# Optimization experiments

Measured on AMD Instinct MI355X. Metric: run time of the kernel, lower is better.

## Reference

```python
import jax, jax.numpy as jnp
import numpy as np

B, W, N, F_IN = 2, 8, 10000, 5
E = 80000
H = 128


def setup_inputs() -> dict:
    key = jax.random.key(0)
    ks = jax.random.split(key, 16)
    s = 0.05
    inp = {
        "x": jax.random.normal(ks[0], (B, W, N, F_IN), dtype=jnp.float32),
        "edge_index": jax.random.randint(ks[1], (2, E), 0, N, dtype=jnp.int64),
        # GCN layer 1 (in_features -> hidden) and layer 2 (hidden -> hidden)
        "gcn1_w": jax.random.normal(ks[2], (F_IN, H), dtype=jnp.float32) * s,
        "gcn1_b": jnp.zeros((H,), dtype=jnp.float32),
        "gcn2_w": jax.random.normal(ks[3], (H, H), dtype=jnp.float32) * s,
        "gcn2_b": jnp.zeros((H,), dtype=jnp.float32),
        # LSTM (torch gate order: i, f, g, o)
        "lstm_w_ih": jax.random.normal(ks[4], (4 * H, H), dtype=jnp.float32) * s,
        "lstm_w_hh": jax.random.normal(ks[5], (4 * H, H), dtype=jnp.float32) * s,
        "lstm_b_ih": jnp.zeros((4 * H,), dtype=jnp.float32),
        "lstm_b_hh": jnp.zeros((4 * H,), dtype=jnp.float32),
        # Decoder MLP: H -> H//2 -> 1
        "dec_w1": jax.random.normal(ks[6], (H, H // 2), dtype=jnp.float32) * s,
        "dec_b1": jnp.zeros((H // 2,), dtype=jnp.float32),
        "dec_w2": jax.random.normal(ks[7], (H // 2, 1), dtype=jnp.float32) * s,
        "dec_b2": jnp.zeros((1,), dtype=jnp.float32),
    }
    return inp


def _forward(x, edge_index, gcn1_w, gcn1_b, gcn2_w, gcn2_b,
             lstm_w_ih, lstm_w_hh, lstm_b_ih, lstm_b_hh,
             dec_w1, dec_b1, dec_w2, dec_b2):
    b, w, n, f_in = x.shape
    h_dim = gcn1_w.shape[1]
    # --- GCN normalization (PyG GCNConv default: add self-loops, sym-norm) ---
    loop = jnp.arange(n, dtype=edge_index.dtype)
    src = jnp.concatenate([edge_index[0], loop])
    dst = jnp.concatenate([edge_index[1], loop])
    deg = jnp.zeros((n,), x.dtype).at[dst].add(jnp.float32(1.0))
    dinv = jax.lax.rsqrt(deg)
    norm = dinv[src] * dinv[dst]  # (E+N,)

    def gcn(h, wm, bias):
        # h: (BW, N, Fin) -> (BW, N, H). Transform-then-aggregate (linear op).
        ht = h @ wm                                   # (BW, N, H)
        msg = ht[:, src, :] * norm[None, :, None]      # (BW, E+N, H)
        agg = jnp.zeros_like(ht).at[:, dst, :].add(msg)
        return agg + bias

    xf = x.reshape(b * w, n, f_in)
    h = jax.nn.relu(gcn(xf, gcn1_w, gcn1_b))   # dropout is identity at eval
    h = jax.nn.relu(gcn(h, gcn2_w, gcn2_b))

    # (BW, N, H) -> (B, N, W, H) -> (B*N, W, H): per-node temporal sequences
    h = h.reshape(b, w, n, h_dim).transpose(0, 2, 1, 3).reshape(b * n, w, h_dim)

    # --- single-layer LSTM, keep only last hidden state ---
    def step(carry, xt):
        hp, cp = carry
        gates = xt @ lstm_w_ih.T + hp @ lstm_w_hh.T + lstm_b_ih + lstm_b_hh
        i, f, g, o = jnp.split(gates, 4, axis=-1)
        c = jax.nn.sigmoid(f) * cp + jax.nn.sigmoid(i) * jnp.tanh(g)
        hn = jax.nn.sigmoid(o) * jnp.tanh(c)
        return (hn, c), None

    init = (jnp.zeros((b * n, h_dim), x.dtype), jnp.zeros((b * n, h_dim), x.dtype))
    (h_last, _), _ = jax.lax.scan(step, init, h.transpose(1, 0, 2))  # scan over W

    # --- MLP decoder ---
    d = jax.nn.relu(h_last @ dec_w1 + dec_b1)
    pred = (d @ dec_w2 + dec_b2)[..., 0]
    return pred.reshape(b, n)


def reference(x, edge_index, gcn1_w, gcn1_b, gcn2_w, gcn2_b,
              lstm_w_ih, lstm_w_hh, lstm_b_ih, lstm_b_hh,
              dec_w1, dec_b1, dec_w2, dec_b2):
    return _forward(x, edge_index, gcn1_w, gcn1_b, gcn2_w, gcn2_b,
                    lstm_w_ih, lstm_w_hh, lstm_b_ih, lstm_b_hh,
                    dec_w1, dec_b1, dec_w2, dec_b2)
```

## Files before the change

### kernel.cpp

```cpp
#include <hip/hip_runtime.h>
#include <hip/hip_fp16.h>
#include <cstdint>
#include <cstddef>

#define Bn   2
#define Wn   8
#define Nn   10000
#define Fin  5
#define En   80000
#define Hn   128
#define BWn  (Bn*Wn)
#define ROWS (BWn*Nn)
#define MR   (Bn*Nn)
#define LROWS 32

typedef _Float16 half8 __attribute__((ext_vector_type(8)));
typedef float f32x4 __attribute__((ext_vector_type(4)));

#define LOG2E 1.44269504088896f

__device__ __forceinline__ float fast_sigmoid(float x) {
    return __builtin_amdgcn_rcpf(1.f + __builtin_amdgcn_exp2f(-LOG2E * x));
}
__device__ __forceinline__ float fast_tanh(float x) {
    return fmaf(-2.f, __builtin_amdgcn_rcpf(1.f + __builtin_amdgcn_exp2f(2.f * LOG2E * x)), 1.f);
}


__global__ void init_counts_kernel(int* counts) {
    int i = blockIdx.x * blockDim.x + threadIdx.x;
    if (i < Nn) counts[i] = 1;
}

__global__ void count_edges_kernel(const int* __restrict__ ei, int* counts) {
    int e = blockIdx.x * blockDim.x + threadIdx.x;
    if (e < En) atomicAdd(&counts[ei[En + e]], 1);
}

enum { CHUNK = 10 };
static_assert(CHUNK * 1024 >= Nn, "scan chunk");

__global__ __launch_bounds__(1024) void scan_kernel(
    const int* __restrict__ counts, int* __restrict__ row_ptr,
    int* __restrict__ fill_ptr, float* __restrict__ dinv) {
    __shared__ int sums[1024];
    const int t = threadIdx.x;
    const int base = t * CHUNK;
    int cnt[CHUNK];
    int s = 0;
    #pragma unroll
    for (int i = 0; i < CHUNK; ++i) {
        int idx = base + i;
        int v = (idx < Nn) ? counts[idx] : 0;
        cnt[i] = v; s += v;
    }
    sums[t] = s;
    __syncthreads();
    for (int off = 1; off < 1024; off <<= 1) {
        int v = (t >= off) ? sums[t - off] : 0;
        __syncthreads();
        sums[t] += v;
        __syncthreads();
    }
    int excl = (t == 0) ? 0 : sums[t - 1];
    #pragma unroll
    for (int i = 0; i < CHUNK; ++i) {
        int idx = base + i;
        if (idx < Nn) {
            row_ptr[idx] = excl;
            fill_ptr[idx] = excl;
            dinv[idx] = rsqrtf((float)cnt[i]);
            excl += cnt[i];
        }
    }
    if (t == 1023) row_ptr[Nn] = excl;
}

__global__ void fill_kernel(const int* __restrict__ ei,
                            const float* __restrict__ dinv,
                            int* fill_ptr, int* __restrict__ col,
                            float* __restrict__ wgt) {
    int i = blockIdx.x * blockDim.x + threadIdx.x;
    if (i < Nn) {
        int p = atomicAdd(&fill_ptr[i], 1);
        col[p] = i;
        wgt[p] = dinv[i] * dinv[i];
    } else if (i < Nn + En) {
        int e = i - Nn;
        int s = ei[e];
        int d = ei[En + e];
        int p = atomicAdd(&fill_ptr[d], 1);
        col[p] = s;
        wgt[p] = dinv[s] * dinv[d];
    }
}


__global__ void bsum_kernel(const float* __restrict__ a, const float* __restrict__ b,
                            float* __restrict__ out) {
    int i = blockIdx.x * blockDim.x + threadIdx.x;
    if (i < 4 * Hn) out[i] = a[i] + b[i];
}

__global__ void convert_w_kernel(const float* __restrict__ wih, const float* __restrict__ whh,
                                 const float* __restrict__ g2w,
                                 _Float16* __restrict__ wif, _Float16* __restrict__ whf,
                                 _Float16* __restrict__ g2wt) {
    int i = blockIdx.x * blockDim.x + threadIdx.x;
    if (i < 131072) {
        int idx = i & 65535;
        int j = idx & 7, lane = (idx >> 3) & 63, kt = (idx >> 9) & 3, ct = idx >> 11;
        int n = ct * 16 + (lane & 15);
        int k = kt * 32 + (lane >> 4) * 8 + j;
        if (i < 65536) wif[idx] = (_Float16)wih[n * 128 + k];
        else           whf[idx] = (_Float16)whh[n * 128 + k];
    } else if (i < 131072 + 16384) {
        int j = i - 131072;
        int n = j >> 7, k = j & 127;
        g2wt[j] = (_Float16)g2w[k * Hn + n];
    }
}

__global__ __launch_bounds__(128) void agg_x_kernel(
    const float* __restrict__ x, const int* __restrict__ row_ptr,
    const int* __restrict__ col, const float* __restrict__ wgt,
    float* __restrict__ aggx) {
    const int n = blockIdx.x;
    const int t = threadIdx.x;
    const int s = t >> 3, f = t & 7;
    if (f >= Fin) return;
    const int start = row_ptr[n], end = row_ptr[n + 1];
    float acc = 0.f;
    for (int e = start; e < end; ++e) {
        int c = col[e];
        acc = fmaf(wgt[e], x[((size_t)s * Nn + c) * Fin + f], acc);
    }
    aggx[((size_t)n * BWn + s) * Fin + f] = acc;
}

__global__ __launch_bounds__(256) void gcn2_fused_kernel(
    const float* __restrict__ aggx, const float* __restrict__ w1,
    const float* __restrict__ b1, const _Float16* __restrict__ g2wt,
    _Float16* __restrict__ C) {
    __shared__ __align__(16) _Float16 s_buf[128][136];
    __shared__ _Float16 Bs[128][40];
    const int tid = threadIdx.x;
    const int m0 = blockIdx.x * 128;
    {
        const int rg = tid >> 4;
        const int cg = tid & 15;
        float wreg[Fin][8], breg[8];
        #pragma unroll
        for (int k = 0; k < 8; ++k) breg[k] = b1[cg * 8 + k];
        #pragma unroll
        for (int f = 0; f < Fin; ++f)
            #pragma unroll
            for (int k = 0; k < 8; ++k) wreg[f][k] = w1[f * Hn + cg * 8 + k];
        #pragma unroll
        for (int rr = 0; rr < 8; ++rr) {
            const float* ar = aggx + (size_t)(m0 + rg * 8 + rr) * Fin;
            float a[Fin];
            #pragma unroll
            for (int f = 0; f < Fin; ++f) a[f] = ar[f];
            half8 v;
            #pragma unroll
            for (int k = 0; k < 8; ++k) {
                float s = breg[k];
                #pragma unroll
                for (int f = 0; f < Fin; ++f) s = fmaf(a[f], wreg[f][k], s);
                v[k] = (_Float16)fmaxf(s, 0.f);
            }
            *(half8*)&s_buf[rg * 8 + rr][cg * 8] = v;
        }
    }
    __syncthreads();
    const int wave = tid >> 6, lane = tid & 63;
    const int l = lane & 15, q = lane >> 4;
    const int wm = (wave & 1) * 64, wn = (wave >> 1) * 64;
    f32x4 acc[4][4];
    #pragma unroll
    for (int i = 0; i < 4; ++i)
        #pragma unroll
        for (int j = 0; j < 4; ++j) acc[i][j] = (f32x4){0.f, 0.f, 0.f, 0.f};
    for (int kt = 0; kt < 128; kt += 32) {
        #pragma unroll
        for (int j = 0; j < 2; ++j) {
            int idx = tid + j * 256;
            int r = idx >> 2, c = (idx & 3) * 8;
            *(half8*)&Bs[r][c] = *(const half8*)(g2wt + (size_t)r * 128 + kt + c);
        }
        __syncthreads();
        half8 af[4], bf[4];
        #pragma unroll
        for (int i = 0; i < 4; ++i) af[i] = *(const half8*)&s_buf[wm + i * 16 + l][kt + q * 8];
        #pragma unroll
        for (int j = 0; j < 4; ++j) bf[j] = *(const half8*)&Bs[wn + j * 16 + l][q * 8];
        #pragma unroll
        for (int i = 0; i < 4; ++i)
            #pragma unroll
            for (int j = 0; j < 4; ++j)
                acc[i][j] = __builtin_amdgcn_mfma_f32_16x16x32_f16(
                    af[i], bf[j], acc[i][j], 0, 0, 0);
        __syncthreads();
    }
    #pragma unroll
    for (int j = 0; j < 4; ++j) {
        int ccol = wn + j * 16 + l;
        #pragma unroll
        for (int i = 0; i < 4; ++i)
            #pragma unroll
            for (int r = 0; r < 4; ++r)
                s_buf[wm + i * 16 + q * 4 + r][ccol] = (_Float16)acc[i][j][r];
    }
    __syncthreads();
    const size_t base = (size_t)m0 * 128;
    #pragma unroll
    for (int it = 0; it < 8; ++it) {
        int idx = it * 256 + tid;
        int row = idx >> 4, ch = (idx & 15) * 8;
        *(half8*)(C + base + (size_t)row * 128 + ch) = *(const half8*)&s_buf[row][ch];
    }
}

__global__ __launch_bounds__(256) void gcn_agg2_kernel(
    const _Float16* __restrict__ ht, const int* __restrict__ row_ptr,
    const int* __restrict__ col, const float* __restrict__ wgt,
    const float* __restrict__ bias, _Float16* __restrict__ out) {
    const int n = blockIdx.x;
    const int t = threadIdx.x;
    const int s = t >> 4;
    const int g = (t & 15) * 8;
    const int start = row_ptr[n], end = row_ptr[n + 1];
    float acc[8];
    #pragma unroll
    for (int j = 0; j < 8; ++j) acc[j] = 0.f;
    for (int e = start; e < end; ++e) {
        const int c = col[e];
        const float w = wgt[e];
        half8 v = *(const half8*)(ht + ((size_t)c * BWn + s) * Hn + g);
        #pragma unroll
        for (int j = 0; j < 8; ++j) acc[j] = fmaf(w, (float)v[j], acc[j]);
    }
    half8 o;
    #pragma unroll
    for (int j = 0; j < 8; ++j) o[j] = (_Float16)fmaxf(acc[j] + bias[g + j], 0.f);
    *(half8*)(out + ((size_t)n * BWn + s) * Hn + g) = o;
}

__global__ __launch_bounds__(512, 1) void lstm_fused2_kernel(
    const _Float16* __restrict__ h2, const _Float16* __restrict__ wif,
    const _Float16* __restrict__ whf, const float* __restrict__ bsum,
    _Float16* __restrict__ hf) {
    __shared__ __align__(16) _Float16 x_lds[2][LROWS][144];
    __shared__ __align__(16) _Float16 h_lds[LROWS][144];
    const int tid = threadIdx.x;
    const int nw = tid >> 6, lane = tid & 63;
    const int l = lane & 15, q = lane >> 4;
    const int r0 = blockIdx.x * LROWS;
    const int srow = tid >> 4, sch = (tid & 15) * 8;
    const int sgrow = r0 + srow;
    const int sb = (sgrow >= Nn) ? 1 : 0;
    const int sn = sgrow - sb * Nn;
    const _Float16* xbase = h2 + ((size_t)sn * BWn + sb * Wn) * 128 + sch;

    half8 wic[4][4], whc[4][4];
    #pragma unroll
    for (int g = 0; g < 4; ++g) {
        int ct = g * 8 + nw;
        #pragma unroll
        for (int kt = 0; kt < 4; ++kt) {
            wic[g][kt] = *(const half8*)(wif + (((size_t)ct * 4 + kt) * 64 + lane) * 8);
            whc[g][kt] = *(const half8*)(whf + (((size_t)ct * 4 + kt) * 64 + lane) * 8);
        }
    }
    float bias[4];
    #pragma unroll
    for (int g = 0; g < 4; ++g) bias[g] = bsum[g * 128 + nw * 16 + l];
    float c_reg[2][4];
    #pragma unroll
    for (int i = 0; i < 2; ++i)
        #pragma unroll
        for (int r = 0; r < 4; ++r) c_reg[i][r] = 0.f;

    *(half8*)&x_lds[0][srow][sch] = *(const half8*)(xbase);
    __syncthreads();

    for (int t = 0; t < Wn; ++t) {
        half8 xv = {0, 0, 0, 0, 0, 0, 0, 0};
        if (t + 1 < Wn) xv = *(const half8*)(xbase + (size_t)(t + 1) * 128);

        f32x4 acc[2][4];
        #pragma unroll
        for (int i = 0; i < 2; ++i)
            #pragma unroll
            for (int g = 0; g < 4; ++g)
                acc[i][g] = (f32x4){bias[g], bias[g], bias[g], bias[g]};

        #pragma unroll
        for (int kt = 0; kt < 4; ++kt) {
            half8 af[2];
            #pragma unroll
            for (int i = 0; i < 2; ++i)
                af[i] = *(const half8*)&x_lds[t & 1][i * 16 + l][kt * 32 + q * 8];
            #pragma unroll
            for (int i = 0; i < 2; ++i)
                #pragma unroll
                for (int g = 0; g < 4; ++g)
                    acc[i][g] = __builtin_amdgcn_mfma_f32_16x16x32_f16(
                        af[i], wic[g][kt], acc[i][g], 0, 0, 0);
        }
        if (t > 0) {
            #pragma unroll
            for (int kt = 0; kt < 4; ++kt) {
                half8 af[2];
                #pragma unroll
                for (int i = 0; i < 2; ++i)
                    af[i] = *(const half8*)&h_lds[i * 16 + l][kt * 32 + q * 8];
                #pragma unroll
                for (int i = 0; i < 2; ++i)
                    #pragma unroll
                    for (int g = 0; g < 4; ++g)
                        acc[i][g] = __builtin_amdgcn_mfma_f32_16x16x32_f16(
                            af[i], whc[g][kt], acc[i][g], 0, 0, 0);
            }
        }
        __syncthreads();

        #pragma unroll
        for (int i = 0; i < 2; ++i) {
            #pragma unroll
            for (int r = 0; r < 4; ++r) {
                float si = fast_sigmoid(acc[i][0][r]);
                float sf = fast_sigmoid(acc[i][1][r]);
                float tg = fast_tanh(acc[i][2][r]);
                float so = fast_sigmoid(acc[i][3][r]);
                float cn = sf * c_reg[i][r] + si * tg;
                c_reg[i][r] = cn;
                h_lds[i * 16 + q * 4 + r][nw * 16 + l] = (_Float16)(so * fast_tanh(cn));
            }
        }
        if (t + 1 < Wn) *(half8*)&x_lds[(t + 1) & 1][srow][sch] = xv;
        __syncthreads();
    }
    *(half8*)(hf + (size_t)sgrow * 128 + sch) = *(const half8*)&h_lds[srow][sch];
}

__global__ __launch_bounds__(256) void decoder_kernel(
    const _Float16* __restrict__ h, const float* __restrict__ w1,
    const float* __restrict__ b1, const float* __restrict__ w2,
    const float* __restrict__ b2, float* __restrict__ out) {
    const int wave = threadIdx.x >> 6;
    const int lane = threadIdx.x & 63;
    const int row = blockIdx.x * 4 + wave;
    if (row >= MR) return;
    const _Float16* hr = h + (size_t)row * Hn;
    float d = b1[lane];
    #pragma unroll 8
    for (int k = 0; k < Hn; ++k) d = fmaf((float)hr[k], w1[k * 64 + lane], d);
    d = fmaxf(d, 0.f);
    float p = d * w2[lane];
    #pragma unroll
    for (int off = 32; off; off >>= 1) p += __shfl_down(p, off);
    if (lane == 0) out[row] = p + b2[0];
}


extern "C" void kernel_launch(void* const* d_in, const int* in_sizes, int n_in,
                              void* d_out, int out_size, void* d_ws, size_t ws_size,
                              hipStream_t stream) {
    const float* x   = (const float*)d_in[0];
    const int*   ei  = (const int*)d_in[1];
    const float* g1w = (const float*)d_in[2];
    const float* g1b = (const float*)d_in[3];
    const float* g2w = (const float*)d_in[4];
    const float* g2b = (const float*)d_in[5];
    const float* wih = (const float*)d_in[6];
    const float* whh = (const float*)d_in[7];
    const float* bih = (const float*)d_in[8];
    const float* bhh = (const float*)d_in[9];
    const float* dw1 = (const float*)d_in[10];
    const float* db1 = (const float*)d_in[11];
    const float* dw2 = (const float*)d_in[12];
    const float* db2 = (const float*)d_in[13];
    float* out = (float*)d_out;

    char* p = (char*)d_ws;
    auto alloc = [&](size_t bytes) {
        char* r = p;
        p += (bytes + 255) & ~(size_t)255;
        return r;
    };
    int*      counts   = (int*)     alloc(Nn * 4);
    int*      row_ptr  = (int*)     alloc((Nn + 1) * 4);
    int*      fill_ptr = (int*)     alloc((Nn + 1) * 4);
    float*    dinv     = (float*)   alloc(Nn * 4);
    float*    bsum     = (float*)   alloc(4 * Hn * 4);
    int*      col      = (int*)     alloc((En + Nn) * 4);
    float*    wgt      = (float*)   alloc((En + Nn) * 4);
    _Float16* wif      = (_Float16*)alloc(512 * 128 * 2);
    _Float16* whf      = (_Float16*)alloc(512 * 128 * 2);
    _Float16* g2wt     = (_Float16*)alloc(128 * 128 * 2);
    float*    aggx     = (float*)   alloc((size_t)ROWS * Fin * 4);
    _Float16* htf      = (_Float16*)alloc((size_t)ROWS * Hn * 2);
    _Float16* h2f      = (_Float16*)alloc((size_t)ROWS * Hn * 2);
    _Float16* hf       = (_Float16*)alloc((size_t)MR * Hn * 2);

    init_counts_kernel<<<(Nn + 255) / 256, 256, 0, stream>>>(counts);
    count_edges_kernel<<<(En + 255) / 256, 256, 0, stream>>>(ei, counts);
    scan_kernel<<<1, 1024, 0, stream>>>(counts, row_ptr, fill_ptr, dinv);
    fill_kernel<<<(Nn + En + 255) / 256, 256, 0, stream>>>(ei, dinv, fill_ptr, col, wgt);
    bsum_kernel<<<(4 * Hn + 255) / 256, 256, 0, stream>>>(bih, bhh, bsum);
    convert_w_kernel<<<(131072 + 16384 + 255) / 256, 256, 0, stream>>>(
        wih, whh, g2w, wif, whf, g2wt);

    agg_x_kernel<<<Nn, 128, 0, stream>>>(x, row_ptr, col, wgt, aggx);

    gcn2_fused_kernel<<<ROWS / 128, 256, 0, stream>>>(aggx, g1w, g1b, g2wt, htf);

    gcn_agg2_kernel<<<Nn, 256, 0, stream>>>(htf, row_ptr, col, wgt, g2b, h2f);

    lstm_fused2_kernel<<<MR / LROWS, 512, 0, stream>>>(h2f, wif, whf, bsum, hf);

    decoder_kernel<<<(MR + 3) / 4, 256, 0, stream>>>(hf, dw1, db1, dw2, db2, out);
}
```

Baseline: 281.7 us.

## Merge setup kernels, transpose x node-major, fuse decoder into LSTM

Four small setup kernels (count init, edge counting, bias sum, weight conversion) become one multi-role setup_kernel plus a memset. The self-loop +1 now happens inside the scan. The setup kernel also transposes x into a node-major layout, so agg_x gathers one contiguous 80-float row per neighbour instead of 16 strided rows. The LSTM double-buffers h_lds to drop one barrier per timestep and runs the MLP decoder in its epilogue, which removes the hf round-trip and one launch. The costs are more LDS in the LSTM kernel and an extra xt buffer in memory.

```diff
diff --git a/kernel.cpp b/kernel.cpp
--- a/kernel.cpp
+++ b/kernel.cpp
@@ -26,15 +26,47 @@
     return fmaf(-2.f, __builtin_amdgcn_rcpf(1.f + __builtin_amdgcn_exp2f(2.f * LOG2E * x)), 1.f);
 }
 
-
-__global__ void init_counts_kernel(int* counts) {
-    int i = blockIdx.x * blockDim.x + threadIdx.x;
-    if (i < Nn) counts[i] = 1;
-}
-
-__global__ void count_edges_kernel(const int* __restrict__ ei, int* counts) {
-    int e = blockIdx.x * blockDim.x + threadIdx.x;
-    if (e < En) atomicAdd(&counts[ei[En + e]], 1);
+__global__ __launch_bounds__(256) void setup_kernel(
+    const int* __restrict__ ei, const float* __restrict__ bih, const float* __restrict__ bhh,
+    const float* __restrict__ wih, const float* __restrict__ whh,
+    const float* __restrict__ g2w, const float* __restrict__ x,
+    int* __restrict__ counts, float* __restrict__ bsum,
+    _Float16* __restrict__ wif, _Float16* __restrict__ whf,
+    _Float16* __restrict__ g2wt, float* __restrict__ xt) {
+    __shared__ float buf[6400];
+    const int b = blockIdx.x;
+    const int tid = threadIdx.x;
+    if (b < 313) {
+        int e = b * 256 + tid;
+        if (e < En) atomicAdd(&counts[ei[En + e]], 1);
+    } else if (b < 315) {
+        int i = (b - 313) * 256 + tid;
+        if (i < 4 * Hn) bsum[i] = bih[i] + bhh[i];
+    } else if (b < 891) {
+        int i = (b - 315) * 256 + tid;
+        if (i < 131072) {
+            int idx = i & 65535;
+            int j = idx & 7, lane = (idx >> 3) & 63, kt = (idx >> 9) & 3, ct = idx >> 11;
+            int n = ct * 16 + (lane & 15);
+            int k = kt * 32 + (lane >> 4) * 8 + j;
+            if (i < 65536) wif[idx] = (_Float16)wih[n * 128 + k];
+            else           whf[idx] = (_Float16)whh[n * 128 + k];
+        } else {
+            int j = i - 131072;
+            int n = j >> 7, k = j & 127;
+            g2wt[j] = (_Float16)g2w[k * Hn + n];
+        }
+    } else {
+        const int n0 = (b - 891) * 80;
+        for (int i = tid; i < 6400; i += 256) {
+            int s = i / 400, r = i - s * 400;
+            int node = r / 5, f = r - node * 5;
+            buf[(node * 16 + s) * 5 + f] = x[((size_t)s * Nn + n0) * 5 + r];
+        }
+        __syncthreads();
+        float* dst = xt + (size_t)n0 * 80;
+        for (int i = tid; i < 6400; i += 256) dst[i] = buf[i];
+    }
 }
 
 enum { CHUNK = 10 };
@@ -51,7 +83,7 @@
     #pragma unroll
     for (int i = 0; i < CHUNK; ++i) {
         int idx = base + i;
-        int v = (idx < Nn) ? counts[idx] : 0;
+        int v = (idx < Nn) ? counts[idx] + 1 : 0;
         cnt[i] = v; s += v;
     }
     sums[t] = s;
@@ -95,34 +127,8 @@
     }
 }
 
-
-__global__ void bsum_kernel(const float* __restrict__ a, const float* __restrict__ b,
-                            float* __restrict__ out) {
-    int i = blockIdx.x * blockDim.x + threadIdx.x;
-    if (i < 4 * Hn) out[i] = a[i] + b[i];
-}
-
-__global__ void convert_w_kernel(const float* __restrict__ wih, const float* __restrict__ whh,
-                                 const float* __restrict__ g2w,
-                                 _Float16* __restrict__ wif, _Float16* __restrict__ whf,
-                                 _Float16* __restrict__ g2wt) {
-    int i = blockIdx.x * blockDim.x + threadIdx.x;
-    if (i < 131072) {
-        int idx = i & 65535;
-        int j = idx & 7, lane = (idx >> 3) & 63, kt = (idx >> 9) & 3, ct = idx >> 11;
-        int n = ct * 16 + (lane & 15);
-        int k = kt * 32 + (lane >> 4) * 8 + j;
-        if (i < 65536) wif[idx] = (_Float16)wih[n * 128 + k];
-        else           whf[idx] = (_Float16)whh[n * 128 + k];
-    } else if (i < 131072 + 16384) {
-        int j = i - 131072;
-        int n = j >> 7, k = j & 127;
-        g2wt[j] = (_Float16)g2w[k * Hn + n];
-    }
-}
-
 __global__ __launch_bounds__(128) void agg_x_kernel(
-    const float* __restrict__ x, const int* __restrict__ row_ptr,
+    const float* __restrict__ xt, const int* __restrict__ row_ptr,
     const int* __restrict__ col, const float* __restrict__ wgt,
     float* __restrict__ aggx) {
     const int n = blockIdx.x;
@@ -130,12 +136,11 @@
     const int s = t >> 3, f = t & 7;
     if (f >= Fin) return;
     const int start = row_ptr[n], end = row_ptr[n + 1];
+    const int off = s * 5 + f;
     float acc = 0.f;
-    for (int e = start; e < end; ++e) {
-        int c = col[e];
-        acc = fmaf(wgt[e], x[((size_t)s * Nn + c) * Fin + f], acc);
-    }
-    aggx[((size_t)n * BWn + s) * Fin + f] = acc;
+    for (int e = start; e < end; ++e)
+        acc = fmaf(wgt[e], xt[(size_t)col[e] * 80 + off], acc);
+    aggx[(size_t)n * 80 + off] = acc;
 }
 
 __global__ __launch_bounds__(256) void gcn2_fused_kernel(
@@ -247,12 +252,14 @@
     *(half8*)(out + ((size_t)n * BWn + s) * Hn + g) = o;
 }
 
-__global__ __launch_bounds__(512, 1) void lstm_fused2_kernel(
+__global__ __launch_bounds__(512, 1) void lstm_fused3_kernel(
     const _Float16* __restrict__ h2, const _Float16* __restrict__ wif,
     const _Float16* __restrict__ whf, const float* __restrict__ bsum,
-    _Float16* __restrict__ hf) {
+    const float* __restrict__ dw1, const float* __restrict__ db1,
+    const float* __restrict__ dw2, const float* __restrict__ db2,
+    float* __restrict__ out) {
     __shared__ __align__(16) _Float16 x_lds[2][LROWS][144];
-    __shared__ __align__(16) _Float16 h_lds[LROWS][144];
+    __shared__ __align__(16) _Float16 h_lds[2][LROWS][144];
     const int tid = threadIdx.x;
     const int nw = tid >> 6, lane = tid & 63;
     const int l = lane & 15, q = lane >> 4;
@@ -315,7 +322,7 @@
                 half8 af[2];
                 #pragma unroll
                 for (int i = 0; i < 2; ++i)
-                    af[i] = *(const half8*)&h_lds[i * 16 + l][kt * 32 + q * 8];
+                    af[i] = *(const half8*)&h_lds[t & 1][i * 16 + l][kt * 32 + q * 8];
                 #pragma unroll
                 for (int i = 0; i < 2; ++i)
                     #pragma unroll
@@ -324,8 +331,6 @@
                             af[i], whc[g][kt], acc[i][g], 0, 0, 0);
             }
         }
-        __syncthreads();
-
         #pragma unroll
         for (int i = 0; i < 2; ++i) {
             #pragma unroll
@@ -336,32 +341,31 @@
                 float so = fast_sigmoid(acc[i][3][r]);
                 float cn = sf * c_reg[i][r] + si * tg;
                 c_reg[i][r] = cn;
-                h_lds[i * 16 + q * 4 + r][nw * 16 + l] = (_Float16)(so * fast_tanh(cn));
+                h_lds[(t + 1) & 1][i * 16 + q * 4 + r][nw * 16 + l] =
+                    (_Float16)(so * fast_tanh(cn));
             }
         }
         if (t + 1 < Wn) *(half8*)&x_lds[(t + 1) & 1][srow][sch] = xv;
         __syncthreads();
     }
-    *(half8*)(hf + (size_t)sgrow * 128 + sch) = *(const half8*)&h_lds[srow][sch];
-}
-
-__global__ __launch_bounds__(256) void decoder_kernel(
-    const _Float16* __restrict__ h, const float* __restrict__ w1,
-    const float* __restrict__ b1, const float* __restrict__ w2,
-    const float* __restrict__ b2, float* __restrict__ out) {
-    const int wave = threadIdx.x >> 6;
-    const int lane = threadIdx.x & 63;
-    const int row = blockIdx.x * 4 + wave;
-    if (row >= MR) return;
-    const _Float16* hr = h + (size_t)row * Hn;
-    float d = b1[lane];
-    #pragma unroll 8
-    for (int k = 0; k < Hn; ++k) d = fmaf((float)hr[k], w1[k * 64 + lane], d);
-    d = fmaxf(d, 0.f);
-    float p = d * w2[lane];
-    #pragma unroll
-    for (int off = 32; off; off >>= 1) p += __shfl_down(p, off);
-    if (lane == 0) out[row] = p + b2[0];
+
+    #pragma unroll
+    for (int rr = 0; rr < 4; ++rr) {
+        const int row = nw + rr * 8;
+        float d = db1[lane];
+        #pragma unroll
+        for (int k8 = 0; k8 < 16; ++k8) {
+            half8 hv = *(const half8*)&h_lds[0][row][k8 * 8];
+            #pragma unroll
+            for (int j = 0; j < 8; ++j)
+                d = fmaf((float)hv[j], dw1[(k8 * 8 + j) * 64 + lane], d);
+        }
+        d = fmaxf(d, 0.f);
+        float p = d * dw2[lane];
+        #pragma unroll
+        for (int off = 32; off; off >>= 1) p += __shfl_down(p, off);
+        if (lane == 0) out[r0 + row] = p + db2[0];
+    }
 }
 
 
@@ -400,26 +404,24 @@
     _Float16* wif      = (_Float16*)alloc(512 * 128 * 2);
     _Float16* whf      = (_Float16*)alloc(512 * 128 * 2);
     _Float16* g2wt     = (_Float16*)alloc(128 * 128 * 2);
+    float*    xt       = (float*)   alloc((size_t)Nn * 80 * 4);
     float*    aggx     = (float*)   alloc((size_t)ROWS * Fin * 4);
     _Float16* htf      = (_Float16*)alloc((size_t)ROWS * Hn * 2);
     _Float16* h2f      = (_Float16*)alloc((size_t)ROWS * Hn * 2);
-    _Float16* hf       = (_Float16*)alloc((size_t)MR * Hn * 2);
-
-    init_counts_kernel<<<(Nn + 255) / 256, 256, 0, stream>>>(counts);
-    count_edges_kernel<<<(En + 255) / 256, 256, 0, stream>>>(ei, counts);
+
+    hipMemsetAsync(counts, 0, Nn * 4, stream);
+
+    setup_kernel<<<1016, 256, 0, stream>>>(ei, bih, bhh, wih, whh, g2w, x,
+                                           counts, bsum, wif, whf, g2wt, xt);
     scan_kernel<<<1, 1024, 0, stream>>>(counts, row_ptr, fill_ptr, dinv);
     fill_kernel<<<(Nn + En + 255) / 256, 256, 0, stream>>>(ei, dinv, fill_ptr, col, wgt);
-    bsum_kernel<<<(4 * Hn + 255) / 256, 256, 0, stream>>>(bih, bhh, bsum);
-    convert_w_kernel<<<(131072 + 16384 + 255) / 256, 256, 0, stream>>>(
-        wih, whh, g2w, wif, whf, g2wt);
-
-    agg_x_kernel<<<Nn, 128, 0, stream>>>(x, row_ptr, col, wgt, aggx);
+
+    agg_x_kernel<<<Nn, 128, 0, stream>>>(xt, row_ptr, col, wgt, aggx);
 
     gcn2_fused_kernel<<<ROWS / 128, 256, 0, stream>>>(aggx, g1w, g1b, g2wt, htf);
 
     gcn_agg2_kernel<<<Nn, 256, 0, stream>>>(htf, row_ptr, col, wgt, g2b, h2f);
 
-    lstm_fused2_kernel<<<MR / LROWS, 512, 0, stream>>>(h2f, wif, whf, bsum, hf);
-
-    decoder_kernel<<<(MR + 3) / 4, 256, 0, stream>>>(hf, dw1, db1, dw2, db2, out);
-}
+    lstm_fused3_kernel<<<MR / LROWS, 512, 0, stream>>>(
+        h2f, wif, whf, bsum, dw1, db1, dw2, db2, out);
+}
```

New measurement: 291.3 us. 1.03x slower.
